# Performance work log

Hardware: AMD Instinct MI355X
Metric: run time of the kernel (lower is better)

Reference implementation:

```python
import jax, jax.numpy as jnp
import numpy as np

B, S, E, H, EMB, V = 64, 2048, 1024, 512, 256, 50257
PAD = 0


def setup_inputs() -> dict:
    key = jax.random.key(0)
    ks = jax.random.split(key, 20)
    inp = {
        "enc_out": jax.random.normal(ks[0], (B, S, E), jnp.float32),
        "h0": jax.random.normal(ks[1], (B, H), jnp.float32),
        "c0": jax.random.normal(ks[2], (B, H), jnp.float32),
        "dec_input": jax.random.randint(ks[3], (B, 1), 0, V),
        "enc_inputs": jax.random.randint(ks[4], (B, S), 0, V),
    }
    s = 0.02
    emb = jax.random.normal(ks[5], (V, EMB), jnp.float32) * s
    inp["embed_table"] = emb.at[PAD].set(0.0)  # padding_idx row zero
    inp["attn_wh_w"] = jax.random.normal(ks[6], (H, E), jnp.float32) * s
    inp["attn_wh_b"] = jnp.zeros((H,), jnp.float32)
    inp["attn_ws_w"] = jax.random.normal(ks[7], (H, H), jnp.float32) * s
    inp["attn_ws_b"] = jnp.zeros((H,), jnp.float32)
    inp["attn_v"] = jax.random.uniform(ks[8], (H,), jnp.float32)
    inp["lstm_w_ih"] = jax.random.normal(ks[9], (4 * H, EMB + E), jnp.float32) * s
    inp["lstm_w_hh"] = jax.random.normal(ks[10], (4 * H, H), jnp.float32) * s
    inp["lstm_b_ih"] = jnp.zeros((4 * H,), jnp.float32)
    inp["lstm_b_hh"] = jnp.zeros((4 * H,), jnp.float32)
    inp["wh_vec"] = jax.random.uniform(ks[11], (E,), jnp.float32)
    inp["ws_vec"] = jax.random.uniform(ks[12], (H,), jnp.float32)
    inp["wx_vec"] = jax.random.uniform(ks[13], (EMB,), jnp.float32)
    inp["v_w"] = jax.random.normal(ks[14], (V, H), jnp.float32) * s
    inp["v_b"] = jnp.zeros((V,), jnp.float32)
    return inp


def _decoder_step(enc_out, h0, c0, dec_input, enc_inputs, embed_table,
                  attn_wh_w, attn_wh_b, attn_ws_w, attn_ws_b, attn_v,
                  lstm_w_ih, lstm_w_hh, lstm_b_ih, lstm_b_hh,
                  wh_vec, ws_vec, wx_vec, v_w, v_b):
    b = enc_out.shape[0]
    # --- attention ---
    wh_app = jnp.einsum('bse,he->bsh', enc_out, attn_wh_w) + attn_wh_b   # [B,S,H]
    ws_app = (h0 @ attn_ws_w.T + attn_ws_b)[:, None, :]                  # [B,1,H]
    energy = jnp.tanh(wh_app + ws_app) @ attn_v                          # [B,S]
    attn = jax.nn.softmax(energy, axis=1)                                # [B,S]
    # --- context + embed ---
    context = jnp.einsum('bs,bse->be', attn, enc_out)                    # [B,E]
    embed = embed_table[dec_input[:, 0]]                                 # [B,EMB]
    x = jnp.concatenate([context, embed], axis=1)                        # [B,E+EMB]
    # --- LSTMCell (torch gate order i,f,g,o) ---
    gates = x @ lstm_w_ih.T + lstm_b_ih + h0 @ lstm_w_hh.T + lstm_b_hh   # [B,4H]
    i, f, g, o = jnp.split(gates, 4, axis=1)
    c_t = jax.nn.sigmoid(f) * c0 + jax.nn.sigmoid(i) * jnp.tanh(g)
    h_t = jax.nn.sigmoid(o) * jnp.tanh(c_t)
    # --- pointer-generator mix ---
    p_vocab = jax.nn.softmax(h_t @ v_w.T + v_b, axis=1)                  # [B,V]
    p_gen = jax.nn.sigmoid(context @ wh_vec + h_t @ ws_vec + embed @ wx_vec)[:, None]  # [B,1]
    attn_scores = jnp.zeros((b, v_w.shape[0]), p_vocab.dtype)
    attn_scores = attn_scores.at[jnp.arange(b)[:, None], enc_inputs].add(attn)
    output = p_gen * p_vocab + (1.0 - p_gen) * attn_scores
    return output, h_t, c_t


def reference(enc_out, h0, c0, dec_input, enc_inputs, embed_table,
              attn_wh_w, attn_wh_b, attn_ws_w, attn_ws_b, attn_v,
              lstm_w_ih, lstm_w_hh, lstm_b_ih, lstm_b_hh,
              wh_vec, ws_vec, wx_vec, v_w, v_b):
    return _decoder_step(enc_out, h0, c0, dec_input, enc_inputs, embed_table,
                         attn_wh_w, attn_wh_b, attn_ws_w, attn_ws_b, attn_v,
                         lstm_w_ih, lstm_w_hh, lstm_b_ih, lstm_b_hh,
                         wh_vec, ws_vec, wx_vec, v_w, v_b)
```

## Files before the change

kernel.cpp:

```cpp
#include <hip/hip_runtime.h>

#define B_   64
#define S_   2048
#define E_   1024
#define H_   512
#define EMB_ 256
#define V_   50257
#define M_   (B_*S_)

typedef __attribute__((ext_vector_type(8))) short bf16x8;
typedef __attribute__((ext_vector_type(4))) float f32x4;

__device__ __forceinline__ unsigned short f2bf(float f) {
  unsigned int u = __float_as_uint(f);
  u += 0x7fffu + ((u >> 16) & 1u);
  return (unsigned short)(u >> 16);
}
__device__ __forceinline__ unsigned pk2(float a, float b) {
  return (unsigned)f2bf(a) | ((unsigned)f2bf(b) << 16);
}
__device__ __forceinline__ float sigm(float x)  { return 1.f / (1.f + __expf(-x)); }
__device__ __forceinline__ float tanh_f(float x){ return 1.f - 2.f / (1.f + __expf(2.f * x)); }

__global__ __launch_bounds__(256) void k_convw(const float* __restrict__ w,
                                               unsigned short* __restrict__ wb) {
  int i = blockIdx.x * 256 + threadIdx.x;
  int byte = i << 1;
  int kt = byte >> 16;
  int r1 = byte & 65535;
  int nc = r1 >> 15;
  int r2 = r1 & 32767;
  int np = r2 >> 7;
  int sb = r2 & 127;
  int kb = sb ^ ((np & 7) << 4);
  int n = nc * 256 + np;
  int k = kt * 64 + (kb >> 1);
  wb[i] = f2bf(w[((size_t)n << 10) + k]);
}

__global__ __launch_bounds__(256) void k_wsapp(const float* __restrict__ h0,
                                               const float* __restrict__ wsw,
                                               const float* __restrict__ wsb,
                                               const float* __restrict__ whb,
                                               float* __restrict__ outw) {
  int g = blockIdx.x * 256 + threadIdx.x;
  int b = g >> 9, n = g & 511;
  const float* hr = h0 + b * 512;
  const float* wr = wsw + (size_t)n * 512;
  float acc = 0.f;
  for (int k = 0; k < 512; k += 4) {
    float4 a = *(const float4*)(hr + k);
    float4 w = *(const float4*)(wr + k);
    acc += a.x*w.x + a.y*w.y + a.z*w.z + a.w*w.w;
  }
  outw[g] = acc + wsb[n] + whb[n];
}

__global__ __launch_bounds__(512, 4) void k_energy(
    const float* __restrict__ enc, const unsigned short* __restrict__ Wb,
    const float* __restrict__ wsb, const float* __restrict__ av,
    float* __restrict__ ep)
{
  __shared__ __attribute__((aligned(16))) char lds[81920];

  const int tid = threadIdx.x;
  const int w = tid >> 6, lane = tid & 63, lr = lane & 15, lg = lane >> 4;
  const int wm = w >> 2, wn = w & 3;
  const int bid = blockIdx.x;
  const int x = bid & 7;
  const int g = bid >> 3;
  const int nc = g & 1;
  const int mt = (g >> 1) * 8 + x;
  const int m0 = mt * 64;
  const int bb = m0 >> 11;

  f32x4 acc[2][4];
  #pragma unroll
  for (int i = 0; i < 2; ++i)
    #pragma unroll
    for (int j = 0; j < 4; ++j)
      #pragma unroll
      for (int r = 0; r < 4; ++r) acc[i][j][r] = 0.f;

  const int arow = tid >> 3, ae = tid & 7;
  const float* aptr = enc + ((size_t)(m0 + arow) << 10) + ae * 8;
  const int aswz = (arow & 7) << 4;

  float4 ar[2];
  auto issueA = [&](int kt) {
    const float* ap = aptr + kt * 64;
    ar[0] = *(const float4*)ap;
    ar[1] = *(const float4*)(ap + 4);
  };
  auto stageA = [&](int d) {
    uint4 pv;
    pv.x = pk2(ar[0].x, ar[0].y); pv.y = pk2(ar[0].z, ar[0].w);
    pv.z = pk2(ar[1].x, ar[1].y); pv.w = pk2(ar[1].z, ar[1].w);
    *(uint4*)(lds + d * 8192 + arow * 128 + ((ae * 16) ^ aswz)) = pv;
  };
  auto gllB = [&](int kt, int d) {
    const char* gp = (const char*)Wb + kt * 65536 + nc * 32768 + w * 4096 + lane * 16;
    char* l = lds + 16384 + d * 32768 + w * 4096 + lane * 16;
    #pragma unroll
    for (int i = 0; i < 4; ++i)
      __builtin_amdgcn_global_load_lds(
          (const __attribute__((address_space(1))) unsigned int*)(gp + i * 1024),
          (__attribute__((address_space(3))) unsigned int*)(l + i * 1024),
          16, 0, 0);
  };

  const int swz = (lr & 7) << 4;
  int abase[2];
  #pragma unroll
  for (int fm = 0; fm < 2; ++fm) abase[fm] = (wm * 32 + fm * 16 + lr) * 128;
  int boff[4];
  #pragma unroll
  for (int fn = 0; fn < 4; ++fn) boff[fn] = 16384 + (wn * 64 + fn * 16 + lr) * 128;

  issueA(0);
  gllB(0, 0);
  stageA(0);
  __syncthreads();

  for (int kt = 0; kt < 16; ++kt) {
    const int buf = kt & 1;
    if (kt < 15) {
      issueA(kt + 1);
      gllB(kt + 1, buf ^ 1);
    }
    const int abuf = buf * 8192;
    const int bbuf = buf * 32768;
    #pragma unroll
    for (int ks = 0; ks < 2; ++ks) {
      const int ko = (ks * 64 + lg * 16) ^ swz;
      bf16x8 af[2];
      #pragma unroll
      for (int fm = 0; fm < 2; ++fm) af[fm] = *(const bf16x8*)(lds + abuf + abase[fm] + ko);
      #pragma unroll
      for (int fn = 0; fn < 4; ++fn) {
        bf16x8 bf = *(const bf16x8*)(lds + bbuf + boff[fn] + ko);
        #pragma unroll
        for (int fm = 0; fm < 2; ++fm)
          acc[fm][fn] = __builtin_amdgcn_mfma_f32_16x16x32_bf16(af[fm], bf, acc[fm][fn], 0, 0, 0);
      }
    }
    if (kt < 15) stageA(buf ^ 1);
    __syncthreads();
  }

  float cw_[4], cv_[4];
  #pragma unroll
  for (int fn = 0; fn < 4; ++fn) {
    int col = nc * 256 + wn * 64 + fn * 16 + lr;
    cw_[fn] = wsb[bb * 512 + col];
    cv_[fn] = av[col];
  }
  float* red = (float*)lds;
  #pragma unroll
  for (int fm = 0; fm < 2; ++fm) {
    #pragma unroll
    for (int r = 0; r < 4; ++r) {
      float v = 0.f;
      #pragma unroll
      for (int fn = 0; fn < 4; ++fn)
        v += cv_[fn] * tanh_f(acc[fm][fn][r] + cw_[fn]);
      v += __shfl_xor(v, 1); v += __shfl_xor(v, 2);
      v += __shfl_xor(v, 4); v += __shfl_xor(v, 8);
      if (lr == 0) red[wn * 64 + wm * 32 + fm * 16 + lg * 4 + r] = v;
    }
  }
  __syncthreads();
  if (tid < 64)
    ep[(size_t)nc * M_ + m0 + tid] = red[tid] + red[64 + tid] + red[128 + tid] + red[192 + tid];
}

__global__ __launch_bounds__(256) void k_attnsm(const float* __restrict__ ep,
                                                float* __restrict__ attn) {
  int b = blockIdx.x, tid = threadIdx.x;
  __shared__ float sm[256];
  float ev[8]; float mx = -3.0e38f;
  #pragma unroll
  for (int i = 0; i < 8; ++i) {
    int m = b * 2048 + i * 256 + tid;
    float v = ep[m] + ep[M_ + m];
    ev[i] = v; mx = fmaxf(mx, v);
  }
  sm[tid] = mx; __syncthreads();
  for (int st = 128; st; st >>= 1) { if (tid < st) sm[tid] = fmaxf(sm[tid], sm[tid + st]); __syncthreads(); }
  mx = sm[0]; __syncthreads();
  float sum = 0.f;
  #pragma unroll
  for (int i = 0; i < 8; ++i) { ev[i] = __expf(ev[i] - mx); sum += ev[i]; }
  sm[tid] = sum; __syncthreads();
  for (int st = 128; st; st >>= 1) { if (tid < st) sm[tid] += sm[tid + st]; __syncthreads(); }
  float inv = 1.f / sm[0];
  #pragma unroll
  for (int i = 0; i < 8; ++i) attn[b * 2048 + i * 256 + tid] = ev[i] * inv;
}

__global__ __launch_bounds__(256) void k_ctx(const float* __restrict__ enc,
                                             const float* __restrict__ attn,
                                             float* __restrict__ cp) {
  int sc = blockIdx.x, b = blockIdx.y, tid = threadIdx.x;
  int e0 = tid * 4;
  float ax = 0.f, ay = 0.f, az = 0.f, aw = 0.f;
  const float* base = enc + (((size_t)b * 2048 + sc * 64) << 10) + e0;
  const float* awt = attn + b * 2048 + sc * 64;
  #pragma unroll 8
  for (int s = 0; s < 64; ++s) {
    float wv = awt[s];
    float4 v = *(const float4*)(base + ((size_t)s << 10));
    ax += wv * v.x; ay += wv * v.y; az += wv * v.z; aw += wv * v.w;
  }
  float4 o; o.x = ax; o.y = ay; o.z = az; o.w = aw;
  *(float4*)(cp + ((size_t)sc * 64 + b) * 1024 + e0) = o;
}

__global__ __launch_bounds__(256) void k_xprep(const float* __restrict__ cp,
                                               const float* __restrict__ et,
                                               const int* __restrict__ dec,
                                               const float* __restrict__ h0,
                                               const float* __restrict__ whv,
                                               const float* __restrict__ wxv,
                                               float* __restrict__ xb,
                                               float* __restrict__ cw) {
  int b = blockIdx.x, tid = threadIdx.x;
  __shared__ float sm[256];
  float acc = 0.f;
  for (int j = tid; j < 1024; j += 256) {
    float s = 0.f;
    #pragma unroll
    for (int sc = 0; sc < 32; ++sc) s += cp[((size_t)sc * 64 + b) * 1024 + j];
    xb[b * 1792 + j] = s;
    acc += s * whv[j];
  }
  int e = dec[b];
  {
    int j = tid;
    float s = et[(size_t)e * 256 + j];
    xb[b * 1792 + 1024 + j] = s;
    acc += s * wxv[j];
  }
  for (int j = tid; j < 512; j += 256)
    xb[b * 1792 + 1280 + j] = h0[b * 512 + j];
  sm[tid] = acc; __syncthreads();
  for (int st = 128; st; st >>= 1) { if (tid < st) sm[tid] += sm[tid + st]; __syncthreads(); }
  if (!tid) cw[b] = sm[0];
}

__global__ __launch_bounds__(256, 2) void k_gates(const float* __restrict__ wih,
                                                  const float* __restrict__ whh,
                                                  const float* __restrict__ xb,
                                                  float* __restrict__ gp) {
  __shared__ __attribute__((aligned(16))) char Bs[56 * 1040];
  const int tid = threadIdx.x;
  const int w = tid >> 6, lane = tid & 63, lr = lane & 15, lg = lane >> 4;
  const int j0 = blockIdx.x * 64;
  const int sl = blockIdx.y;
  const int k0 = sl * 448;

  #pragma unroll
  for (int i = 0; i < 16; ++i) {
    int slot = i * 256 + tid;
    int kq = slot & 63, n = slot >> 6;
    if (kq < 56) {
      const float4* p = (const float4*)(xb + n * 1792 + k0 + kq * 8);
      float4 x0 = p[0], x1 = p[1];
      uint4 pv;
      pv.x = pk2(x0.x, x0.y); pv.y = pk2(x0.z, x0.w);
      pv.z = pk2(x1.x, x1.y); pv.w = pk2(x1.z, x1.w);
      *(uint4*)(Bs + kq * 1040 + n * 16) = pv;
    }
  }
  __syncthreads();

  f32x4 acc[4];
  #pragma unroll
  for (int fn = 0; fn < 4; ++fn)
    #pragma unroll
    for (int r = 0; r < 4; ++r) acc[fn][r] = 0.f;

  const int j = j0 + w * 16 + lr;
  for (int ks = 0; ks < 14; ++ks) {
    int kg = k0 + ks * 32 + lg * 8;
    const float* ap = (kg < 1280) ? (wih + (size_t)j * 1280 + kg)
                                  : (whh + (size_t)j * 512 + (kg - 1280));
    float4 x0 = *(const float4*)ap, x1 = *(const float4*)(ap + 4);
    bf16x8 af;
    unsigned* au = (unsigned*)&af;
    au[0] = pk2(x0.x, x0.y); au[1] = pk2(x0.z, x0.w);
    au[2] = pk2(x1.x, x1.y); au[3] = pk2(x1.z, x1.w);
    #pragma unroll
    for (int fn = 0; fn < 4; ++fn) {
      bf16x8 bf = *(const bf16x8*)(Bs + (ks * 4 + lg) * 1040 + (fn * 16 + lr) * 16);
      acc[fn] = __builtin_amdgcn_mfma_f32_16x16x32_bf16(af, bf, acc[fn], 0, 0, 0);
    }
  }
  #pragma unroll
  for (int fn = 0; fn < 4; ++fn) {
    int b = fn * 16 + lr;
    #pragma unroll
    for (int r = 0; r < 4; ++r) {
      int jr = j0 + w * 16 + lg * 4 + r;
      gp[((size_t)sl * 64 + b) * 2048 + jr] = acc[fn][r];
    }
  }
}

__global__ __launch_bounds__(512) void k_lstm(const float* __restrict__ gp,
                                              const float* __restrict__ bih,
                                              const float* __restrict__ bhh,
                                              const float* __restrict__ c0,
                                              const float* __restrict__ cw,
                                              const float* __restrict__ wsv,
                                              float* __restrict__ dout,
                                              float* __restrict__ pg) {
  int b = blockIdx.x, h = threadIdx.x;
  __shared__ float sm[512];
  float gi = bih[h]        + bhh[h];
  float gf = bih[512 + h]  + bhh[512 + h];
  float gg = bih[1024 + h] + bhh[1024 + h];
  float go = bih[1536 + h] + bhh[1536 + h];
  #pragma unroll
  for (int kc = 0; kc < 4; ++kc) {
    const float* g = gp + ((size_t)kc * 64 + b) * 2048;
    gi += g[h]; gf += g[512 + h]; gg += g[1024 + h]; go += g[1536 + h];
  }
  float c  = sigm(gf) * c0[b * 512 + h] + sigm(gi) * tanh_f(gg);
  float ht = sigm(go) * tanh_f(c);
  dout[(size_t)B_ * V_ + b * 512 + h] = ht;
  dout[(size_t)B_ * V_ + B_ * H_ + b * 512 + h] = c;
  sm[h] = ht * wsv[h];
  __syncthreads();
  for (int st = 256; st; st >>= 1) { if (h < st) sm[h] += sm[h + st]; __syncthreads(); }
  if (!h) pg[b] = sigm(cw[b] + sm[0]);
}

__global__ __launch_bounds__(256, 2) void k_logits(const float* __restrict__ vw,
                                                   const float* __restrict__ vb,
                                                   const float* __restrict__ ht,
                                                   float* __restrict__ out) {
  __shared__ __attribute__((aligned(16))) char Bs[64 * 1040];
  const int tid = threadIdx.x;
  const int w = tid >> 6, lane = tid & 63, lr = lane & 15, lg = lane >> 4;
  const int v0 = blockIdx.x * 128;

  #pragma unroll
  for (int i = 0; i < 16; ++i) {
    int slot = i * 256 + tid;
    int kq = slot & 63, n = slot >> 6;
    const float4* p = (const float4*)(ht + n * 512 + kq * 8);
    float4 x0 = p[0], x1 = p[1];
    uint4 pv;
    pv.x = pk2(x0.x, x0.y); pv.y = pk2(x0.z, x0.w);
    pv.z = pk2(x1.x, x1.y); pv.w = pk2(x1.z, x1.w);
    *(uint4*)(Bs + kq * 1040 + n * 16) = pv;
  }
  __syncthreads();

  f32x4 acc[2][4];
  #pragma unroll
  for (int fm = 0; fm < 2; ++fm)
    #pragma unroll
    for (int fn = 0; fn < 4; ++fn)
      #pragma unroll
      for (int r = 0; r < 4; ++r) acc[fm][fn][r] = 0.f;

  int row0 = v0 + w * 32 + lr;
  int row1 = row0 + 16;
  const float* a0p = vw + (size_t)min(row0, V_ - 1) * 512 + lg * 8;
  const float* a1p = vw + (size_t)min(row1, V_ - 1) * 512 + lg * 8;

  float4 pa0[2], pa1[2];
  pa0[0] = *(const float4*)a0p; pa0[1] = *(const float4*)(a0p + 4);
  pa1[0] = *(const float4*)a1p; pa1[1] = *(const float4*)(a1p + 4);

  for (int ks = 0; ks < 16; ++ks) {
    bf16x8 af0, af1;
    {
      unsigned* u = (unsigned*)&af0;
      u[0] = pk2(pa0[0].x, pa0[0].y); u[1] = pk2(pa0[0].z, pa0[0].w);
      u[2] = pk2(pa0[1].x, pa0[1].y); u[3] = pk2(pa0[1].z, pa0[1].w);
      unsigned* v = (unsigned*)&af1;
      v[0] = pk2(pa1[0].x, pa1[0].y); v[1] = pk2(pa1[0].z, pa1[0].w);
      v[2] = pk2(pa1[1].x, pa1[1].y); v[3] = pk2(pa1[1].z, pa1[1].w);
    }
    if (ks < 15) {
      const float* n0 = a0p + (ks + 1) * 32;
      const float* n1 = a1p + (ks + 1) * 32;
      pa0[0] = *(const float4*)n0; pa0[1] = *(const float4*)(n0 + 4);
      pa1[0] = *(const float4*)n1; pa1[1] = *(const float4*)(n1 + 4);
    }
    const char* bbase = Bs + (ks * 4 + lg) * 1040 + lr * 16;
    #pragma unroll
    for (int fn = 0; fn < 4; ++fn) {
      bf16x8 bf = *(const bf16x8*)(bbase + fn * 256);
      acc[0][fn] = __builtin_amdgcn_mfma_f32_16x16x32_bf16(af0, bf, acc[0][fn], 0, 0, 0);
      acc[1][fn] = __builtin_amdgcn_mfma_f32_16x16x32_bf16(af1, bf, acc[1][fn], 0, 0, 0);
    }
  }

  #pragma unroll
  for (int fm = 0; fm < 2; ++fm) {
    #pragma unroll
    for (int r = 0; r < 4; ++r) {
      int vrow = v0 + w * 32 + fm * 16 + lg * 4 + r;
      if (vrow < V_) {
        float bias = vb[vrow];
        #pragma unroll
        for (int fn = 0; fn < 4; ++fn) {
          int b = fn * 16 + lr;
          out[(size_t)b * V_ + vrow] = acc[fm][fn][r] + bias;
        }
      }
    }
  }
}

#define VCH 6283
__global__ __launch_bounds__(256) void k_sm1(const float* __restrict__ out,
                                             float* __restrict__ pst) {
  int c = blockIdx.x, b = blockIdx.y, tid = threadIdx.x;
  __shared__ float sm[256];
  const float* row = out + (size_t)b * V_;
  int v0 = c * VCH, v1 = min(v0 + VCH, V_);
  float mx = -3.0e38f;
  for (int v = v0 + tid; v < v1; v += 256) mx = fmaxf(mx, row[v]);
  sm[tid] = mx; __syncthreads();
  for (int st = 128; st; st >>= 1) { if (tid < st) sm[tid] = fmaxf(sm[tid], sm[tid + st]); __syncthreads(); }
  mx = sm[0]; __syncthreads();
  float sum = 0.f;
  for (int v = v0 + tid; v < v1; v += 256) sum += __expf(row[v] - mx);
  sm[tid] = sum; __syncthreads();
  for (int st = 128; st; st >>= 1) { if (tid < st) sm[tid] += sm[tid + st]; __syncthreads(); }
  if (!tid) { pst[(b * 8 + c) * 2] = mx; pst[(b * 8 + c) * 2 + 1] = sm[0]; }
}

__global__ __launch_bounds__(64) void k_sm2(const float* __restrict__ pst,
                                            float* __restrict__ stats) {
  int b = threadIdx.x;
  float mx = -3.0e38f;
  #pragma unroll
  for (int c = 0; c < 8; ++c) mx = fmaxf(mx, pst[(b * 8 + c) * 2]);
  float s = 0.f;
  #pragma unroll
  for (int c = 0; c < 8; ++c)
    s += pst[(b * 8 + c) * 2 + 1] * __expf(pst[(b * 8 + c) * 2] - mx);
  stats[b * 2] = mx; stats[b * 2 + 1] = s;
}

__global__ __launch_bounds__(256) void k_final(float* __restrict__ out,
                                               const float* __restrict__ stats,
                                               const float* __restrict__ pg) {
  int v = blockIdx.x * 256 + threadIdx.x;
  int b = blockIdx.y;
  if (v < V_) {
    float mx = stats[b * 2];
    float scale = pg[b] / stats[b * 2 + 1];
    size_t i = (size_t)b * V_ + v;
    out[i] = scale * __expf(out[i] - mx);
  }
}

__global__ __launch_bounds__(256) void k_scatter(float* __restrict__ out,
                                                 const float* __restrict__ attn,
                                                 const int* __restrict__ einp,
                                                 const float* __restrict__ pg) {
  int b = blockIdx.y;
  int s = blockIdx.x * 256 + threadIdx.x;
  int v = einp[b * 2048 + s];
  float w = (1.f - pg[b]) * attn[b * 2048 + s];
  atomicAdd(out + (size_t)b * V_ + v, w);
}

extern "C" void kernel_launch(void* const* d_in, const int* in_sizes, int n_in,
                              void* d_out, int out_size, void* d_ws, size_t ws_size,
                              hipStream_t stream) {
  const float* enc  = (const float*)d_in[0];
  const float* h0   = (const float*)d_in[1];
  const float* c0   = (const float*)d_in[2];
  const int*   dec  = (const int*)d_in[3];
  const int*   einp = (const int*)d_in[4];
  const float* et   = (const float*)d_in[5];
  const float* whw  = (const float*)d_in[6];
  const float* whb  = (const float*)d_in[7];
  const float* wsw  = (const float*)d_in[8];
  const float* wsbv = (const float*)d_in[9];
  const float* av   = (const float*)d_in[10];
  const float* wih  = (const float*)d_in[11];
  const float* whh  = (const float*)d_in[12];
  const float* bih  = (const float*)d_in[13];
  const float* bhh  = (const float*)d_in[14];
  const float* whv  = (const float*)d_in[15];
  const float* wsv  = (const float*)d_in[16];
  const float* wxv  = (const float*)d_in[17];
  const float* vw   = (const float*)d_in[18];
  const float* vb   = (const float*)d_in[19];
  float* out = (float*)d_out;

  char* ws = (char*)d_ws;
  unsigned short* Wb = (unsigned short*)(ws + 0);
  float* wsbt  = (float*)(ws + 1048576);
  float* ep    = (float*)(ws + 1179648);
  float* attn  = (float*)(ws + 2228224);
  float* cpgp  = (float*)(ws + 2752512);
  float* xb    = (float*)(ws + 11141120);
  float* cw    = (float*)(ws + 11599872);
  float* pg    = (float*)(ws + 11600128);
  float* stats = (float*)(ws + 11600384);
  float* pst   = (float*)(ws + 11600896);

  k_convw  <<<2048, 256, 0, stream>>>(whw, Wb);
  k_wsapp  <<<128, 256, 0, stream>>>(h0, wsw, wsbv, whb, wsbt);
  k_energy <<<4096, 512, 0, stream>>>(enc, Wb, wsbt, av, ep);
  k_attnsm <<<64, 256, 0, stream>>>(ep, attn);
  k_ctx    <<<dim3(32, 64), 256, 0, stream>>>(enc, attn, cpgp);
  k_xprep  <<<64, 256, 0, stream>>>(cpgp, et, dec, h0, whv, wxv, xb, cw);
  k_gates  <<<dim3(32, 4), 256, 0, stream>>>(wih, whh, xb, cpgp);
  k_lstm   <<<64, 512, 0, stream>>>(cpgp, bih, bhh, c0, cw, wsv, out, pg);
  k_logits <<<393, 256, 0, stream>>>(vw, vb, out + (size_t)B_ * V_, out);
  k_sm1    <<<dim3(8, 64), 256, 0, stream>>>(out, pst);
  k_sm2    <<<1, 64, 0, stream>>>(pst, stats);
  k_final  <<<dim3(197, 64), 256, 0, stream>>>(out, stats, pg);
  k_scatter<<<dim3(8, 64), 256, 0, stream>>>(out, attn, einp, pg);
}
```

Baseline: 459.7 us.

## Double energy GEMM M-tile and triple-buffer B loads with explicit waitcnt pipeline

```diff
diff --git a/kernel.cpp b/kernel.cpp
--- a/kernel.cpp
+++ b/kernel.cpp
@@ -56,12 +56,12 @@
   outw[g] = acc + wsb[n] + whb[n];
 }
 
-__global__ __launch_bounds__(512, 4) void k_energy(
+__global__ __launch_bounds__(512) void k_energy(
     const float* __restrict__ enc, const unsigned short* __restrict__ Wb,
     const float* __restrict__ wsb, const float* __restrict__ av,
     float* __restrict__ ep)
 {
-  __shared__ __attribute__((aligned(16))) char lds[81920];
+  __shared__ __attribute__((aligned(16))) char lds[131072];
 
   const int tid = threadIdx.x;
   const int w = tid >> 6, lane = tid & 63, lr = lane & 15, lg = lane >> 4;
@@ -71,36 +71,41 @@
   const int g = bid >> 3;
   const int nc = g & 1;
   const int mt = (g >> 1) * 8 + x;
-  const int m0 = mt * 64;
+  const int m0 = mt * 128;
   const int bb = m0 >> 11;
 
-  f32x4 acc[2][4];
-  #pragma unroll
-  for (int i = 0; i < 2; ++i)
+  f32x4 acc[4][4];
+  #pragma unroll
+  for (int i = 0; i < 4; ++i)
     #pragma unroll
     for (int j = 0; j < 4; ++j)
       #pragma unroll
       for (int r = 0; r < 4; ++r) acc[i][j][r] = 0.f;
 
-  const int arow = tid >> 3, ae = tid & 7;
-  const float* aptr = enc + ((size_t)(m0 + arow) << 10) + ae * 8;
+  const int arow = tid >> 2, aq = tid & 3;
+  const float* aptr = enc + ((size_t)(m0 + arow) << 10) + aq * 16;
   const int aswz = (arow & 7) << 4;
 
-  float4 ar[2];
-  auto issueA = [&](int kt) {
+  float4 ar0[4], ar1[4];
+
+  auto issueA = [&](int kt, float4* ar) {
     const float* ap = aptr + kt * 64;
-    ar[0] = *(const float4*)ap;
-    ar[1] = *(const float4*)(ap + 4);
+    #pragma unroll
+    for (int i = 0; i < 4; ++i) ar[i] = *(const float4*)(ap + i * 4);
   };
-  auto stageA = [&](int d) {
-    uint4 pv;
-    pv.x = pk2(ar[0].x, ar[0].y); pv.y = pk2(ar[0].z, ar[0].w);
-    pv.z = pk2(ar[1].x, ar[1].y); pv.w = pk2(ar[1].z, ar[1].w);
-    *(uint4*)(lds + d * 8192 + arow * 128 + ((ae * 16) ^ aswz)) = pv;
+  auto stageA = [&](const float4* ar, int d) {
+    uint4 pv0, pv1;
+    pv0.x = pk2(ar[0].x, ar[0].y); pv0.y = pk2(ar[0].z, ar[0].w);
+    pv0.z = pk2(ar[1].x, ar[1].y); pv0.w = pk2(ar[1].z, ar[1].w);
+    pv1.x = pk2(ar[2].x, ar[2].y); pv1.y = pk2(ar[2].z, ar[2].w);
+    pv1.z = pk2(ar[3].x, ar[3].y); pv1.w = pk2(ar[3].z, ar[3].w);
+    char* ab = lds + d * 16384 + arow * 128;
+    *(uint4*)(ab + ((aq * 32 +  0) ^ aswz)) = pv0;
+    *(uint4*)(ab + ((aq * 32 + 16) ^ aswz)) = pv1;
   };
   auto gllB = [&](int kt, int d) {
     const char* gp = (const char*)Wb + kt * 65536 + nc * 32768 + w * 4096 + lane * 16;
-    char* l = lds + 16384 + d * 32768 + w * 4096 + lane * 16;
+    char* l = lds + 32768 + d * 32768 + w * 4096 + lane * 16;
     #pragma unroll
     for (int i = 0; i < 4; ++i)
       __builtin_amdgcn_global_load_lds(
@@ -110,42 +115,55 @@
   };
 
   const int swz = (lr & 7) << 4;
-  int abase[2];
-  #pragma unroll
-  for (int fm = 0; fm < 2; ++fm) abase[fm] = (wm * 32 + fm * 16 + lr) * 128;
+  int abase[4];
+  #pragma unroll
+  for (int fm = 0; fm < 4; ++fm) abase[fm] = (wm * 64 + fm * 16 + lr) * 128;
   int boff[4];
   #pragma unroll
-  for (int fn = 0; fn < 4; ++fn) boff[fn] = 16384 + (wn * 64 + fn * 16 + lr) * 128;
-
-  issueA(0);
-  gllB(0, 0);
-  stageA(0);
-  __syncthreads();
-
-  for (int kt = 0; kt < 16; ++kt) {
-    const int buf = kt & 1;
-    if (kt < 15) {
-      issueA(kt + 1);
-      gllB(kt + 1, buf ^ 1);
-    }
-    const int abuf = buf * 8192;
-    const int bbuf = buf * 32768;
+  for (int fn = 0; fn < 4; ++fn) boff[fn] = (wn * 64 + fn * 16 + lr) * 128;
+
+  auto step = [&](int kt, float4* arIss, const float4* arStg) {
+    const int tIss = (kt + 2) & 15;
+    issueA(tIss, arIss);
+    gllB(tIss, (kt + 2) % 3);
+    asm volatile("s_waitcnt vmcnt(8)" ::: "memory");
+    __builtin_amdgcn_sched_barrier(0);
+    const int abuf = (kt & 1) * 16384;
+    const char* bbuf = lds + 32768 + (kt % 3) * 32768;
     #pragma unroll
     for (int ks = 0; ks < 2; ++ks) {
       const int ko = (ks * 64 + lg * 16) ^ swz;
-      bf16x8 af[2];
+      bf16x8 af[4];
       #pragma unroll
-      for (int fm = 0; fm < 2; ++fm) af[fm] = *(const bf16x8*)(lds + abuf + abase[fm] + ko);
+      for (int fm = 0; fm < 4; ++fm) af[fm] = *(const bf16x8*)(lds + abuf + abase[fm] + ko);
       #pragma unroll
       for (int fn = 0; fn < 4; ++fn) {
-        bf16x8 bf = *(const bf16x8*)(lds + bbuf + boff[fn] + ko);
+        bf16x8 bf = *(const bf16x8*)(bbuf + boff[fn] + ko);
         #pragma unroll
-        for (int fm = 0; fm < 2; ++fm)
+        for (int fm = 0; fm < 4; ++fm)
           acc[fm][fn] = __builtin_amdgcn_mfma_f32_16x16x32_bf16(af[fm], bf, acc[fm][fn], 0, 0, 0);
       }
     }
-    if (kt < 15) stageA(buf ^ 1);
-    __syncthreads();
+    stageA(arStg, (kt + 1) & 1);
+    asm volatile("s_waitcnt lgkmcnt(0)" ::: "memory");
+    __builtin_amdgcn_sched_barrier(0);
+    __builtin_amdgcn_s_barrier();
+    __builtin_amdgcn_sched_barrier(0);
+  };
+
+  issueA(0, ar0); gllB(0, 0);
+  issueA(1, ar1); gllB(1, 1);
+  asm volatile("s_waitcnt vmcnt(8)" ::: "memory");
+  __builtin_amdgcn_sched_barrier(0);
+  stageA(ar0, 0);
+  asm volatile("s_waitcnt lgkmcnt(0)" ::: "memory");
+  __builtin_amdgcn_sched_barrier(0);
+  __builtin_amdgcn_s_barrier();
+  __builtin_amdgcn_sched_barrier(0);
+
+  for (int kt = 0; kt < 16; kt += 2) {
+    step(kt,     ar0, ar1);
+    step(kt + 1, ar1, ar0);
   }
 
   float cw_[4], cv_[4];
@@ -157,7 +175,7 @@
   }
   float* red = (float*)lds;
   #pragma unroll
-  for (int fm = 0; fm < 2; ++fm) {
+  for (int fm = 0; fm < 4; ++fm) {
     #pragma unroll
     for (int r = 0; r < 4; ++r) {
       float v = 0.f;
@@ -166,12 +184,12 @@
         v += cv_[fn] * tanh_f(acc[fm][fn][r] + cw_[fn]);
       v += __shfl_xor(v, 1); v += __shfl_xor(v, 2);
       v += __shfl_xor(v, 4); v += __shfl_xor(v, 8);
-      if (lr == 0) red[wn * 64 + wm * 32 + fm * 16 + lg * 4 + r] = v;
+      if (lr == 0) red[wn * 128 + wm * 64 + fm * 16 + lg * 4 + r] = v;
     }
   }
   __syncthreads();
-  if (tid < 64)
-    ep[(size_t)nc * M_ + m0 + tid] = red[tid] + red[64 + tid] + red[128 + tid] + red[192 + tid];
+  if (tid < 128)
+    ep[(size_t)nc * M_ + m0 + tid] = red[tid] + red[128 + tid] + red[256 + tid] + red[384 + tid];
 }
 
 __global__ __launch_bounds__(256) void k_attnsm(const float* __restrict__ ep,
@@ -512,7 +530,7 @@
 
   k_convw  <<<2048, 256, 0, stream>>>(whw, Wb);
   k_wsapp  <<<128, 256, 0, stream>>>(h0, wsw, wsbv, whb, wsbt);
-  k_energy <<<4096, 512, 0, stream>>>(enc, Wb, wsbt, av, ep);
+  k_energy <<<2048, 512, 0, stream>>>(enc, Wb, wsbt, av, ep);
   k_attnsm <<<64, 256, 0, stream>>>(ep, attn);
   k_ctx    <<<dim3(32, 64), 256, 0, stream>>>(enc, attn, cpgp);
   k_xprep  <<<64, 256, 0, stream>>>(cpgp, et, dec, h0, whv, wxv, xb, cw);
```

New measurement: 521.4 us. 13.4% more time.
